# Optimization experiments

Measured on AMD Instinct MI355X. Metric: run time of the kernel, lower is better.

## Reference

```python
import jax, jax.numpy as jnp
import numpy as np

OUT_F, IN_F, RANK = 4096, 4096, 32
N_TOK = 8192  # batch 4 * seq 2048, flattened


def setup_inputs() -> dict:
    key = jax.random.key(0)
    k_x, k_w, k_s, k_a, k_b, k_bias = jax.random.split(key, 6)
    x = jax.random.normal(k_x, (N_TOK, IN_F), dtype=jnp.float32)
    # ternary weights in {-1, 0, +1}, stored as int8 buffer
    weight_q = (jax.random.randint(k_w, (OUT_F, IN_F), 0, 3) - 1).astype(jnp.int8)
    # per-output-channel absmean scale, shape [out, 1], positive
    scale = 0.02 + 0.05 * jax.random.uniform(k_s, (OUT_F, 1), dtype=jnp.float32)
    lora_A = 0.01 * jax.random.normal(k_a, (OUT_F, RANK), dtype=jnp.float32)
    lora_B = 0.01 * jax.random.normal(k_b, (RANK, IN_F), dtype=jnp.float32)
    bias = 0.01 * jax.random.normal(k_bias, (OUT_F,), dtype=jnp.float32)
    return {"x": x, "weight_q": weight_q, "scale": scale,
            "lora_A": lora_A, "lora_B": lora_B, "bias": bias}


def reference(x, weight_q, scale, lora_A, lora_B, bias):
    # out = (x @ W_q^T) * scale_per_out_channel + x @ B^T @ A^T + bias
    Wq = weight_q.astype(x.dtype)                       # dequantize {-1,0,1}
    out = jnp.einsum('ti,oi->to', x, Wq) * scale.reshape(1, -1)
    # low-rank LoRA residual: (x @ B^T) @ A^T, rank-RANK bottleneck
    out = out + (x @ lora_B.T) @ lora_A.T
    out = out + bias
    return out
```

## Files before the change

kernel.cpp:

```cpp
#include <hip/hip_runtime.h>
#include <stdint.h>

typedef unsigned short u16;
typedef __attribute__((ext_vector_type(8))) __bf16 bf16x8;
typedef __attribute__((ext_vector_type(4))) float f32x4;

__device__ __forceinline__ u16 f2bf(float f) {
  unsigned int u = __builtin_bit_cast(unsigned int, f);
  u = (u + 0x7FFFu + ((u >> 16) & 1u)) >> 16;
  return (u16)u;
}
__device__ __forceinline__ u16 tern2bf(int s) {
  return s == 0 ? (u16)0 : (s > 0 ? (u16)0x3F80 : (u16)0xBF80);
}

#define GLOAD_LDS16(g, l)                                                          \
  __builtin_amdgcn_global_load_lds((__attribute__((address_space(1))) void*)(g),   \
                                   (__attribute__((address_space(3))) void*)(l),   \
                                   16, 0, 0)

#define M_TOK 8192
#define N_OUT 4096
#define K_IN  4096
#define RANK  32

#define WS_XB    0ull
#define WS_WB    67108864ull
#define WS_BB    100663296ull
#define WS_A32   100925440ull
#define WS_T32   101187584ull
#define WS_TPART 101711872ull
#define WS_FLAG  110100480ull

__global__ void k_convert_x(const float4* __restrict__ x, ushort4* __restrict__ xb, int n4) {
  int stride = gridDim.x * blockDim.x;
  for (int i = blockIdx.x * blockDim.x + threadIdx.x; i < n4; i += stride) {
    float4 v = x[i];
    ushort4 o;
    o.x = f2bf(v.x); o.y = f2bf(v.y); o.z = f2bf(v.z); o.w = f2bf(v.w);
    xb[i] = o;
  }
}

__global__ void k_detect_wtype(const int* __restrict__ w, int* __restrict__ flag) {
  int v = w[threadIdx.x];
  bool ok = (v >= -1 && v <= 1);
  unsigned long long m = __ballot(ok);
  if (threadIdx.x == 0) *flag = (m == ~0ull) ? 1 : 0;
}

__global__ void k_convert_w(const void* __restrict__ wq, const int* __restrict__ flag,
                            ushort4* __restrict__ wb, int n4) {
  int is32 = *flag;
  int stride = gridDim.x * blockDim.x;
  for (int i = blockIdx.x * blockDim.x + threadIdx.x; i < n4; i += stride) {
    int s0, s1, s2, s3;
    if (is32) {
      int4 c = ((const int4*)wq)[i];
      s0 = c.x; s1 = c.y; s2 = c.z; s3 = c.w;
    } else {
      char4 c = ((const char4*)wq)[i];
      s0 = c.x; s1 = c.y; s2 = c.z; s3 = c.w;
    }
    ushort4 o;
    o.x = tern2bf(s0); o.y = tern2bf(s1); o.z = tern2bf(s2); o.w = tern2bf(s3);
    wb[i] = o;
  }
}

__global__ void k_prep_B(const float* __restrict__ loraB, u16* __restrict__ bb) {
  int idx = blockIdx.x * blockDim.x + threadIdx.x;
  if (idx < RANK * K_IN) bb[idx] = f2bf(loraB[idx]);
}

__global__ void k_prep_A(const float* __restrict__ loraA, const float* __restrict__ scale,
                         u16* __restrict__ a32) {
  int idx = blockIdx.x * blockDim.x + threadIdx.x;
  if (idx >= N_OUT * RANK) return;
  int o = idx >> 5;
  a32[idx] = f2bf(loraA[idx] / scale[o]);
}

__global__ __launch_bounds__(256) void k_lora_T(const u16* __restrict__ xb,
                                                const u16* __restrict__ bb,
                                                float* __restrict__ tpart) {
  __shared__ u16 As[256 * 32];
  __shared__ u16 Bs[32 * 32];
  int mt = blockIdx.x >> 3;
  int ks = blockIdx.x & 7;
  int tid = threadIdx.x, lane = tid & 63, wave = tid >> 6;
  int m0 = mt * 256;
  int kbase0 = ks * 512;
  f32x4 acc[4][2] = {};
  for (int step = 0; step < 16; ++step) {
    int kb = kbase0 + step * 32;
    __syncthreads();
#pragma unroll
    for (int i = 0; i < 4; ++i) {
      const u16* src = xb + (size_t)(m0 + i * 64 + (tid >> 2)) * K_IN + kb + (tid & 3) * 8;
      GLOAD_LDS16(src, &As[i * 2048 + tid * 8]);
    }
    if (tid < 128) {
      const u16* src = bb + (size_t)(tid >> 2) * K_IN + kb + (tid & 3) * 8;
      GLOAD_LDS16(src, &Bs[tid * 8]);
    }
    __syncthreads();
    bf16x8 b[2];
#pragma unroll
    for (int ni = 0; ni < 2; ++ni)
      b[ni] = *(const bf16x8*)&Bs[(ni * 16 + (lane & 15)) * 32 + (lane >> 4) * 8];
#pragma unroll
    for (int mi = 0; mi < 4; ++mi) {
      bf16x8 a = *(const bf16x8*)&As[(wave * 64 + mi * 16 + (lane & 15)) * 32 + (lane >> 4) * 8];
      acc[mi][0] = __builtin_amdgcn_mfma_f32_16x16x32_bf16(a, b[0], acc[mi][0], 0, 0, 0);
      acc[mi][1] = __builtin_amdgcn_mfma_f32_16x16x32_bf16(a, b[1], acc[mi][1], 0, 0, 0);
    }
  }
#pragma unroll
  for (int mi = 0; mi < 4; ++mi)
#pragma unroll
    for (int ni = 0; ni < 2; ++ni)
#pragma unroll
      for (int r = 0; r < 4; ++r) {
        int row = m0 + wave * 64 + mi * 16 + (lane >> 4) * 4 + r;
        int col = ni * 16 + (lane & 15);
        tpart[((size_t)ks * M_TOK + row) * RANK + col] = acc[mi][ni][r];
      }
}

__global__ void k_reduce_T(const float* __restrict__ tpart, u16* __restrict__ t32) {
  int idx = blockIdx.x * blockDim.x + threadIdx.x;
  if (idx >= M_TOK * RANK) return;
  int t = idx >> 5, r = idx & 31;
  float v = 0.f;
#pragma unroll
  for (int s = 0; s < 8; ++s) v += tpart[((size_t)s * M_TOK + t) * RANK + r];
  t32[idx] = f2bf(v);
}

__global__ __launch_bounds__(512, 2) void k_gemm8(const u16* __restrict__ xb,
                                                  const u16* __restrict__ wb,
                                                  const u16* __restrict__ t32,
                                                  const u16* __restrict__ a32,
                                                  const float* __restrict__ scale,
                                                  const float* __restrict__ bias,
                                                  float* __restrict__ out) {
  __shared__ u16 As[4][8192];
  __shared__ u16 Bs[4][8192];
  const int tid = threadIdx.x;
  const int l = tid & 63, w = tid >> 6;
  const int wm = w >> 2, wn = w & 3;
  const int bid = blockIdx.x;
  const int swz = (bid & 7) * 64 + (bid >> 3);
  const int m0 = (swz >> 4) * 256, n0 = (swz & 15) * 256;

  const int srow0 = (w * 2 + 0) * 16 + (l >> 2);
  const int srow1 = (w * 2 + 1) * 16 + (l >> 2);
  const int scx = ((l & 3) ^ ((l >> 3) & 3)) * 8;
  const int ldst0 = (w * 2 + 0) * 512 + l * 8;
  const int ldst1 = (w * 2 + 1) * 512 + l * 8;
  const int r15 = l & 15;
  const int cxr = (((l >> 4) ^ ((r15 >> 1) & 3)) * 8);

  f32x4 acc[8][4] = {};

  u16* AsF = &As[0][0];
  u16* BsF = &Bs[0][0];
  const u16* axs0 = xb + (size_t)(m0 + srow0) * K_IN + scx;
  const u16* axs1 = xb + (size_t)(m0 + srow1) * K_IN + scx;
  const u16* bxs0 = wb + (size_t)(n0 + srow0) * K_IN + scx;
  const u16* bxs1 = wb + (size_t)(n0 + srow1) * K_IN + scx;

#pragma unroll
  for (int ts = 0; ts < 3; ++ts) {
    GLOAD_LDS16(axs0 + ts * 32, AsF + ts * 8192 + ldst0);
    GLOAD_LDS16(axs1 + ts * 32, AsF + ts * 8192 + ldst1);
    GLOAD_LDS16(bxs0 + ts * 32, BsF + ts * 8192 + ldst0);
    GLOAD_LDS16(bxs1 + ts * 32, BsF + ts * 8192 + ldst1);
  }
  asm volatile("s_waitcnt vmcnt(8)" ::: "memory");
  asm volatile("s_barrier" ::: "memory");

  const int abase = (wm * 128 + r15) * 32 + cxr;
  const int bbase = (wn * 64 + r15) * 32 + cxr;

  const u16* ap0 = axs0 + 96;
  const u16* ap1 = axs1 + 96;
  const u16* bp0 = bxs0 + 96;
  const u16* bp1 = bxs1 + 96;

#define TILE(SLOT, STAGE_A, STAGE_B, WAIT, BAR)                                     \
  {                                                                                 \
    const u16* Asl = AsF + (SLOT) * 8192;                                           \
    const u16* Bsl = BsF + (SLOT) * 8192;                                           \
    bf16x8 a0[4], bfr[4], a1[4];                                                    \
    _Pragma("unroll") for (int mi = 0; mi < 4; ++mi)                                \
        a0[mi] = *(const bf16x8*)&Asl[abase + mi * 512];                            \
    _Pragma("unroll") for (int nj = 0; nj < 4; ++nj)                                \
        bfr[nj] = *(const bf16x8*)&Bsl[bbase + nj * 512];                           \
    STAGE_A                                                                         \
    __builtin_amdgcn_s_setprio(1);                                                  \
    _Pragma("unroll") for (int mi = 0; mi < 4; ++mi)                                \
    _Pragma("unroll") for (int nj = 0; nj < 4; ++nj)                                \
        acc[mi][nj] =                                                               \
            __builtin_amdgcn_mfma_f32_16x16x32_bf16(a0[mi], bfr[nj], acc[mi][nj], 0, 0, 0); \
    __builtin_amdgcn_s_setprio(0);                                                  \
    _Pragma("unroll") for (int mi = 0; mi < 4; ++mi)                                \
        a1[mi] = *(const bf16x8*)&Asl[abase + 2048 + mi * 512];                     \
    STAGE_B                                                                         \
    WAIT                                                                            \
    __builtin_amdgcn_s_setprio(1);                                                  \
    _Pragma("unroll") for (int mi = 0; mi < 4; ++mi)                                \
    _Pragma("unroll") for (int nj = 0; nj < 4; ++nj)                                \
        acc[4 + mi][nj] =                                                           \
            __builtin_amdgcn_mfma_f32_16x16x32_bf16(a1[mi], bfr[nj], acc[4 + mi][nj], 0, 0, 0); \
    __builtin_amdgcn_s_setprio(0);                                                  \
    BAR                                                                             \
  }

#define SA(DST)                                                                     \
  { GLOAD_LDS16(ap0, AsF + (DST) * 8192 + ldst0);                                   \
    GLOAD_LDS16(ap1, AsF + (DST) * 8192 + ldst1); }
#define SB(DST)                                                                     \
  { GLOAD_LDS16(bp0, BsF + (DST) * 8192 + ldst0);                                   \
    GLOAD_LDS16(bp1, BsF + (DST) * 8192 + ldst1);                                   \
    ap0 += 32; ap1 += 32; bp0 += 32; bp1 += 32; }
#define W8  asm volatile("s_waitcnt vmcnt(8)" ::: "memory");
#define W4  asm volatile("s_waitcnt vmcnt(4)" ::: "memory");
#define W0  asm volatile("s_waitcnt vmcnt(0)" ::: "memory");
#define BARR asm volatile("s_barrier" ::: "memory");

#pragma unroll 1
  for (int t = 0; t < 124; t += 4) {
    TILE(0, SA(3), SB(3), W8, BARR)
    TILE(1, SA(0), SB(0), W8, BARR)
    TILE(2, SA(1), SB(1), W8, BARR)
    TILE(3, SA(2), SB(2), W8, BARR)
  }
  TILE(0, SA(3), SB(3), W8, BARR)
  {
    const u16* la0 = t32 + (size_t)(m0 + srow0) * RANK + scx;
    const u16* la1 = t32 + (size_t)(m0 + srow1) * RANK + scx;
    const u16* lb0 = a32 + (size_t)(n0 + srow0) * RANK + scx;
    const u16* lb1 = a32 + (size_t)(n0 + srow1) * RANK + scx;
    TILE(1,
         { GLOAD_LDS16(la0, AsF + 0 * 8192 + ldst0); GLOAD_LDS16(la1, AsF + 0 * 8192 + ldst1); },
         { GLOAD_LDS16(lb0, BsF + 0 * 8192 + ldst0); GLOAD_LDS16(lb1, BsF + 0 * 8192 + ldst1); },
         W8, BARR)
  }
  TILE(2, , , W4, BARR)
  TILE(3, , , W0, BARR)
  TILE(0, , , , )

#pragma unroll
  for (int nj = 0; nj < 4; ++nj) {
    int col = n0 + wn * 64 + nj * 16 + r15;
    float s = scale[col], bv = bias[col];
#pragma unroll
    for (int fi = 0; fi < 8; ++fi) {
      int row = m0 + wm * 128 + (fi >> 2) * 64 + (fi & 3) * 16 + (l >> 4) * 4;
#pragma unroll
      for (int r = 0; r < 4; ++r)
        out[(size_t)(row + r) * N_OUT + col] = acc[fi][nj][r] * s + bv;
    }
  }
}

extern "C" void kernel_launch(void* const* d_in, const int* in_sizes, int n_in,
                              void* d_out, int out_size, void* d_ws, size_t ws_size,
                              hipStream_t stream) {
  const float* x     = (const float*)d_in[0];
  const void*  wq    = d_in[1];
  const float* scale = (const float*)d_in[2];
  const float* loraA = (const float*)d_in[3];
  const float* loraB = (const float*)d_in[4];
  const float* bias  = (const float*)d_in[5];
  float* out = (float*)d_out;

  char* ws = (char*)d_ws;
  u16*   xb    = (u16*)(ws + WS_XB);
  u16*   wbuf  = (u16*)(ws + WS_WB);
  u16*   bb    = (u16*)(ws + WS_BB);
  u16*   a32   = (u16*)(ws + WS_A32);
  u16*   t32   = (u16*)(ws + WS_T32);
  float* tpart = (float*)(ws + WS_TPART);
  int*   flag  = (int*)(ws + WS_FLAG);

  k_convert_x<<<2048, 256, 0, stream>>>((const float4*)x, (ushort4*)xb, M_TOK * K_IN / 4);
  k_detect_wtype<<<1, 64, 0, stream>>>((const int*)wq, flag);
  k_convert_w<<<2048, 256, 0, stream>>>(wq, flag, (ushort4*)wbuf, N_OUT * K_IN / 4);
  k_prep_B<<<512, 256, 0, stream>>>(loraB, bb);
  k_prep_A<<<512, 256, 0, stream>>>(loraA, scale, a32);
  k_lora_T<<<256, 256, 0, stream>>>(xb, bb, tpart);
  k_reduce_T<<<1024, 256, 0, stream>>>(tpart, t32);
  k_gemm8<<<512, 512, 0, stream>>>(xb, wbuf, t32, a32, scale, bias, out);

  (void)in_sizes; (void)n_in; (void)out_size; (void)ws_size;
}
```

Measured before the change: 325.8 us.

## Load weight B fragments directly into registers, bypassing LDS staging

The weight operand is no longer staged through shared memory. Each wave reads its B fragments straight from global memory into registers, double-buffered one tile ahead, and only the activation tile still goes through the four-slot LDS ring. This halves LDS capacity and traffic and removes the B-side LDS reads, which may allow more occupancy. In exchange, each wave issues its own uncoalesced 16-byte global loads, so waves that share an n-tile duplicate weight fetches, and register pressure rises along with a more fragile vmcnt accounting.

```diff
diff --git a/kernel.cpp b/kernel.cpp
--- a/kernel.cpp
+++ b/kernel.cpp
@@ -146,7 +146,6 @@
                                                   const float* __restrict__ bias,
                                                   float* __restrict__ out) {
   __shared__ u16 As[4][8192];
-  __shared__ u16 Bs[4][8192];
   const int tid = threadIdx.x;
   const int l = tid & 63, w = tid >> 6;
   const int wm = w >> 2, wn = w & 3;
@@ -165,92 +164,93 @@
   f32x4 acc[8][4] = {};
 
   u16* AsF = &As[0][0];
-  u16* BsF = &Bs[0][0];
   const u16* axs0 = xb + (size_t)(m0 + srow0) * K_IN + scx;
   const u16* axs1 = xb + (size_t)(m0 + srow1) * K_IN + scx;
-  const u16* bxs0 = wb + (size_t)(n0 + srow0) * K_IN + scx;
-  const u16* bxs1 = wb + (size_t)(n0 + srow1) * K_IN + scx;
+
+  const u16* wrowp[4];
+#pragma unroll
+  for (int nj = 0; nj < 4; ++nj)
+    wrowp[nj] = wb + (size_t)(n0 + wn * 64 + nj * 16 + r15) * K_IN + (l >> 4) * 8;
+  const u16* arowp[4];
+#pragma unroll
+  for (int nj = 0; nj < 4; ++nj)
+    arowp[nj] = a32 + (size_t)(n0 + wn * 64 + nj * 16 + r15) * RANK + (l >> 4) * 8;
+
+  bf16x8 bA[4], bB[4];
 
 #pragma unroll
   for (int ts = 0; ts < 3; ++ts) {
     GLOAD_LDS16(axs0 + ts * 32, AsF + ts * 8192 + ldst0);
     GLOAD_LDS16(axs1 + ts * 32, AsF + ts * 8192 + ldst1);
-    GLOAD_LDS16(bxs0 + ts * 32, BsF + ts * 8192 + ldst0);
-    GLOAD_LDS16(bxs1 + ts * 32, BsF + ts * 8192 + ldst1);
-  }
-  asm volatile("s_waitcnt vmcnt(8)" ::: "memory");
+  }
+#pragma unroll
+  for (int nj = 0; nj < 4; ++nj) { bA[nj] = *(const bf16x8*)(wrowp[nj]); wrowp[nj] += 32; }
+  asm volatile("s_waitcnt vmcnt(4)" ::: "memory");
   asm volatile("s_barrier" ::: "memory");
 
   const int abase = (wm * 128 + r15) * 32 + cxr;
-  const int bbase = (wn * 64 + r15) * 32 + cxr;
 
   const u16* ap0 = axs0 + 96;
   const u16* ap1 = axs1 + 96;
-  const u16* bp0 = bxs0 + 96;
-  const u16* bp1 = bxs1 + 96;
-
-#define TILE(SLOT, STAGE_A, STAGE_B, WAIT, BAR)                                     \
+
+#define SA(DST)                                                                     \
+  { GLOAD_LDS16(ap0, AsF + (DST) * 8192 + ldst0);                                   \
+    GLOAD_LDS16(ap1, AsF + (DST) * 8192 + ldst1);                                   \
+    ap0 += 32; ap1 += 32; }
+#define LOADB_W(BN)                                                                 \
+  { _Pragma("unroll") for (int nj = 0; nj < 4; ++nj) {                              \
+      BN[nj] = *(const bf16x8*)(wrowp[nj]); wrowp[nj] += 32; } }
+#define LOADB_L(BN)                                                                 \
+  { _Pragma("unroll") for (int nj = 0; nj < 4; ++nj) BN[nj] = *(const bf16x8*)(arowp[nj]); }
+#define W12 asm volatile("s_waitcnt vmcnt(12)" ::: "memory");
+#define W10 asm volatile("s_waitcnt vmcnt(10)" ::: "memory");
+#define W8  asm volatile("s_waitcnt vmcnt(8)" ::: "memory");
+#define BARR asm volatile("s_barrier" ::: "memory");
+
+#define TILE(SLOT, BC, LOADB, STAGE, WAIT, BAR)                                     \
   {                                                                                 \
     const u16* Asl = AsF + (SLOT) * 8192;                                           \
-    const u16* Bsl = BsF + (SLOT) * 8192;                                           \
-    bf16x8 a0[4], bfr[4], a1[4];                                                    \
+    bf16x8 a0[4], a1[4];                                                            \
     _Pragma("unroll") for (int mi = 0; mi < 4; ++mi)                                \
         a0[mi] = *(const bf16x8*)&Asl[abase + mi * 512];                            \
-    _Pragma("unroll") for (int nj = 0; nj < 4; ++nj)                                \
-        bfr[nj] = *(const bf16x8*)&Bsl[bbase + nj * 512];                           \
-    STAGE_A                                                                         \
+    LOADB                                                                           \
+    STAGE                                                                           \
     __builtin_amdgcn_s_setprio(1);                                                  \
     _Pragma("unroll") for (int mi = 0; mi < 4; ++mi)                                \
     _Pragma("unroll") for (int nj = 0; nj < 4; ++nj)                                \
         acc[mi][nj] =                                                               \
-            __builtin_amdgcn_mfma_f32_16x16x32_bf16(a0[mi], bfr[nj], acc[mi][nj], 0, 0, 0); \
+            __builtin_amdgcn_mfma_f32_16x16x32_bf16(a0[mi], BC[nj], acc[mi][nj], 0, 0, 0); \
     __builtin_amdgcn_s_setprio(0);                                                  \
     _Pragma("unroll") for (int mi = 0; mi < 4; ++mi)                                \
         a1[mi] = *(const bf16x8*)&Asl[abase + 2048 + mi * 512];                     \
-    STAGE_B                                                                         \
-    WAIT                                                                            \
     __builtin_amdgcn_s_setprio(1);                                                  \
     _Pragma("unroll") for (int mi = 0; mi < 4; ++mi)                                \
     _Pragma("unroll") for (int nj = 0; nj < 4; ++nj)                                \
         acc[4 + mi][nj] =                                                           \
-            __builtin_amdgcn_mfma_f32_16x16x32_bf16(a1[mi], bfr[nj], acc[4 + mi][nj], 0, 0, 0); \
+            __builtin_amdgcn_mfma_f32_16x16x32_bf16(a1[mi], BC[nj], acc[4 + mi][nj], 0, 0, 0); \
     __builtin_amdgcn_s_setprio(0);                                                  \
+    WAIT                                                                            \
     BAR                                                                             \
   }
-
-#define SA(DST)                                                                     \
-  { GLOAD_LDS16(ap0, AsF + (DST) * 8192 + ldst0);                                   \
-    GLOAD_LDS16(ap1, AsF + (DST) * 8192 + ldst1); }
-#define SB(DST)                                                                     \
-  { GLOAD_LDS16(bp0, BsF + (DST) * 8192 + ldst0);                                   \
-    GLOAD_LDS16(bp1, BsF + (DST) * 8192 + ldst1);                                   \
-    ap0 += 32; ap1 += 32; bp0 += 32; bp1 += 32; }
-#define W8  asm volatile("s_waitcnt vmcnt(8)" ::: "memory");
-#define W4  asm volatile("s_waitcnt vmcnt(4)" ::: "memory");
-#define W0  asm volatile("s_waitcnt vmcnt(0)" ::: "memory");
-#define BARR asm volatile("s_barrier" ::: "memory");
 
 #pragma unroll 1
   for (int t = 0; t < 124; t += 4) {
-    TILE(0, SA(3), SB(3), W8, BARR)
-    TILE(1, SA(0), SB(0), W8, BARR)
-    TILE(2, SA(1), SB(1), W8, BARR)
-    TILE(3, SA(2), SB(2), W8, BARR)
-  }
-  TILE(0, SA(3), SB(3), W8, BARR)
+    TILE(0, bA, LOADB_W(bB), SA(3), W12, BARR)
+    TILE(1, bB, LOADB_W(bA), SA(0), W12, BARR)
+    TILE(2, bA, LOADB_W(bB), SA(1), W12, BARR)
+    TILE(3, bB, LOADB_W(bA), SA(2), W12, BARR)
+  }
+  TILE(0, bA, LOADB_W(bB), SA(3), W12, BARR)
   {
     const u16* la0 = t32 + (size_t)(m0 + srow0) * RANK + scx;
     const u16* la1 = t32 + (size_t)(m0 + srow1) * RANK + scx;
-    const u16* lb0 = a32 + (size_t)(n0 + srow0) * RANK + scx;
-    const u16* lb1 = a32 + (size_t)(n0 + srow1) * RANK + scx;
-    TILE(1,
+    TILE(1, bB, LOADB_W(bA),
          { GLOAD_LDS16(la0, AsF + 0 * 8192 + ldst0); GLOAD_LDS16(la1, AsF + 0 * 8192 + ldst1); },
-         { GLOAD_LDS16(lb0, BsF + 0 * 8192 + ldst0); GLOAD_LDS16(lb1, BsF + 0 * 8192 + ldst1); },
-         W8, BARR)
-  }
-  TILE(2, , , W4, BARR)
-  TILE(3, , , W0, BARR)
-  TILE(0, , , , )
+         W12, BARR)
+  }
+  TILE(2, bA, LOADB_W(bB), , W10, BARR)
+  TILE(3, bB, LOADB_L(bA), , W8, BARR)
+  TILE(0, bA, , , , )
 
 #pragma unroll
   for (int nj = 0; nj < 4; ++nj) {
```

Result: slower. 439.3 us (+34.8%).

## Prefetch next tile's LDS fragments into registers before barrier

Applied to the files above, without the earlier changes.

Restructures the 4-stage LDS ring loop so each tile's first A fragments and B fragments are read from LDS for the next slot at the end of the current tile, after the vmcnt wait and before the barrier. The loads are double-buffered in even/odd register sets. The waitcnt thresholds are retuned to vmcnt(4), and pointer increments are split per operand. The aim is to hide LDS read latency behind the preceding MFMA work. In exchange it uses more VGPRs, which may lower occupancy, and requires careful slot-hazard ordering in the ring.

```diff
diff --git a/kernel.cpp b/kernel.cpp
--- a/kernel.cpp
+++ b/kernel.cpp
@@ -178,7 +178,7 @@
     GLOAD_LDS16(bxs0 + ts * 32, BsF + ts * 8192 + ldst0);
     GLOAD_LDS16(bxs1 + ts * 32, BsF + ts * 8192 + ldst1);
   }
-  asm volatile("s_waitcnt vmcnt(8)" ::: "memory");
+  asm volatile("s_waitcnt vmcnt(4)" ::: "memory");
   asm volatile("s_barrier" ::: "memory");
 
   const int abase = (wm * 128 + r15) * 32 + cxr;
@@ -189,68 +189,74 @@
   const u16* bp0 = bxs0 + 96;
   const u16* bp1 = bxs1 + 96;
 
-#define TILE(SLOT, STAGE_A, STAGE_B, WAIT, BAR)                                     \
+#define SA(DST)                                                                     \
+  { GLOAD_LDS16(ap0, AsF + (DST) * 8192 + ldst0);                                   \
+    GLOAD_LDS16(ap1, AsF + (DST) * 8192 + ldst1);                                   \
+    ap0 += 32; ap1 += 32; }
+#define SB(DST)                                                                     \
+  { GLOAD_LDS16(bp0, BsF + (DST) * 8192 + ldst0);                                   \
+    GLOAD_LDS16(bp1, BsF + (DST) * 8192 + ldst1);                                   \
+    bp0 += 32; bp1 += 32; }
+#define W4  asm volatile("s_waitcnt vmcnt(4)" ::: "memory");
+#define W0  asm volatile("s_waitcnt vmcnt(0)" ::: "memory");
+#define BARR asm volatile("s_barrier" ::: "memory");
+#define READN(NS, A0N, BN)                                                          \
+  { const u16* An = AsF + (NS) * 8192;                                              \
+    const u16* Bn = BsF + (NS) * 8192;                                              \
+    _Pragma("unroll") for (int mi = 0; mi < 4; ++mi)                                \
+        A0N[mi] = *(const bf16x8*)&An[abase + mi * 512];                            \
+    _Pragma("unroll") for (int nj = 0; nj < 4; ++nj)                                \
+        BN[nj] = *(const bf16x8*)&Bn[bbase + nj * 512]; }
+
+#define TILE(SLOT, A0C, BC, STAGE_A, STAGE_B, WAIT, RD, BAR)                        \
   {                                                                                 \
     const u16* Asl = AsF + (SLOT) * 8192;                                           \
-    const u16* Bsl = BsF + (SLOT) * 8192;                                           \
-    bf16x8 a0[4], bfr[4], a1[4];                                                    \
+    bf16x8 a1[4];                                                                   \
     _Pragma("unroll") for (int mi = 0; mi < 4; ++mi)                                \
-        a0[mi] = *(const bf16x8*)&Asl[abase + mi * 512];                            \
-    _Pragma("unroll") for (int nj = 0; nj < 4; ++nj)                                \
-        bfr[nj] = *(const bf16x8*)&Bsl[bbase + nj * 512];                           \
+        a1[mi] = *(const bf16x8*)&Asl[abase + 2048 + mi * 512];                     \
     STAGE_A                                                                         \
     __builtin_amdgcn_s_setprio(1);                                                  \
     _Pragma("unroll") for (int mi = 0; mi < 4; ++mi)                                \
     _Pragma("unroll") for (int nj = 0; nj < 4; ++nj)                                \
         acc[mi][nj] =                                                               \
-            __builtin_amdgcn_mfma_f32_16x16x32_bf16(a0[mi], bfr[nj], acc[mi][nj], 0, 0, 0); \
+            __builtin_amdgcn_mfma_f32_16x16x32_bf16(A0C[mi], BC[nj], acc[mi][nj], 0, 0, 0); \
     __builtin_amdgcn_s_setprio(0);                                                  \
-    _Pragma("unroll") for (int mi = 0; mi < 4; ++mi)                                \
-        a1[mi] = *(const bf16x8*)&Asl[abase + 2048 + mi * 512];                     \
     STAGE_B                                                                         \
-    WAIT                                                                            \
     __builtin_amdgcn_s_setprio(1);                                                  \
     _Pragma("unroll") for (int mi = 0; mi < 4; ++mi)                                \
     _Pragma("unroll") for (int nj = 0; nj < 4; ++nj)                                \
         acc[4 + mi][nj] =                                                           \
-            __builtin_amdgcn_mfma_f32_16x16x32_bf16(a1[mi], bfr[nj], acc[4 + mi][nj], 0, 0, 0); \
+            __builtin_amdgcn_mfma_f32_16x16x32_bf16(a1[mi], BC[nj], acc[4 + mi][nj], 0, 0, 0); \
     __builtin_amdgcn_s_setprio(0);                                                  \
+    WAIT                                                                            \
+    RD                                                                              \
     BAR                                                                             \
   }
 
-#define SA(DST)                                                                     \
-  { GLOAD_LDS16(ap0, AsF + (DST) * 8192 + ldst0);                                   \
-    GLOAD_LDS16(ap1, AsF + (DST) * 8192 + ldst1); }
-#define SB(DST)                                                                     \
-  { GLOAD_LDS16(bp0, BsF + (DST) * 8192 + ldst0);                                   \
-    GLOAD_LDS16(bp1, BsF + (DST) * 8192 + ldst1);                                   \
-    ap0 += 32; ap1 += 32; bp0 += 32; bp1 += 32; }
-#define W8  asm volatile("s_waitcnt vmcnt(8)" ::: "memory");
-#define W4  asm volatile("s_waitcnt vmcnt(4)" ::: "memory");
-#define W0  asm volatile("s_waitcnt vmcnt(0)" ::: "memory");
-#define BARR asm volatile("s_barrier" ::: "memory");
+  bf16x8 a0e[4], be[4], a0o[4], bo[4];
+  READN(0, a0e, be)
 
 #pragma unroll 1
   for (int t = 0; t < 124; t += 4) {
-    TILE(0, SA(3), SB(3), W8, BARR)
-    TILE(1, SA(0), SB(0), W8, BARR)
-    TILE(2, SA(1), SB(1), W8, BARR)
-    TILE(3, SA(2), SB(2), W8, BARR)
-  }
-  TILE(0, SA(3), SB(3), W8, BARR)
+    TILE(0, a0e, be, SA(3), SB(3), W4, READN(1, a0o, bo), BARR)
+    TILE(1, a0o, bo, SA(0), SB(0), W4, READN(2, a0e, be), BARR)
+    TILE(2, a0e, be, SA(1), SB(1), W4, READN(3, a0o, bo), BARR)
+    TILE(3, a0o, bo, SA(2), SB(2), W4, READN(0, a0e, be), BARR)
+  }
+  TILE(0, a0e, be, SA(3), SB(3), W4, READN(1, a0o, bo), BARR)
   {
     const u16* la0 = t32 + (size_t)(m0 + srow0) * RANK + scx;
     const u16* la1 = t32 + (size_t)(m0 + srow1) * RANK + scx;
     const u16* lb0 = a32 + (size_t)(n0 + srow0) * RANK + scx;
     const u16* lb1 = a32 + (size_t)(n0 + srow1) * RANK + scx;
-    TILE(1,
+    TILE(1, a0o, bo,
          { GLOAD_LDS16(la0, AsF + 0 * 8192 + ldst0); GLOAD_LDS16(la1, AsF + 0 * 8192 + ldst1); },
          { GLOAD_LDS16(lb0, BsF + 0 * 8192 + ldst0); GLOAD_LDS16(lb1, BsF + 0 * 8192 + ldst1); },
-         W8, BARR)
-  }
-  TILE(2, , , W4, BARR)
-  TILE(3, , , W0, BARR)
-  TILE(0, , , , )
+         W4, READN(2, a0e, be), BARR)
+  }
+  TILE(2, a0e, be, , , W0, READN(3, a0o, bo), BARR)
+  TILE(3, a0o, bo, , , , READN(0, a0e, be), BARR)
+  TILE(0, a0e, be, , , , , )
 
 #pragma unroll
   for (int nj = 0; nj < 4; ++nj) {
```

Result: no change. 323.3 us (-0.8%).

## Split each K-tile into two barrier-separated phases with explicit LDS waits

Applied to the files above, without the earlier changes.

The per-tile body becomes two phases (PHA and PHB), each ending its LDS fragment loads with an explicit lgkmcnt(0) wait and surrounded by workgroup barriers. This is meant to make waves in the block issue their MFMA bursts in lockstep, in the style of ping-pong scheduling, and to cut register pressure by reusing a single fa/fb fragment set. The cost is extra barriers per tile (four instead of one), which may add stalls and reduce how much LDS reads overlap with MFMA.

```diff
diff --git a/kernel.cpp b/kernel.cpp
--- a/kernel.cpp
+++ b/kernel.cpp
@@ -189,68 +189,81 @@
   const u16* bp0 = bxs0 + 96;
   const u16* bp1 = bxs1 + 96;
 
-#define TILE(SLOT, STAGE_A, STAGE_B, WAIT, BAR)                                     \
-  {                                                                                 \
-    const u16* Asl = AsF + (SLOT) * 8192;                                           \
-    const u16* Bsl = BsF + (SLOT) * 8192;                                           \
-    bf16x8 a0[4], bfr[4], a1[4];                                                    \
-    _Pragma("unroll") for (int mi = 0; mi < 4; ++mi)                                \
-        a0[mi] = *(const bf16x8*)&Asl[abase + mi * 512];                            \
-    _Pragma("unroll") for (int nj = 0; nj < 4; ++nj)                                \
-        bfr[nj] = *(const bf16x8*)&Bsl[bbase + nj * 512];                           \
-    STAGE_A                                                                         \
-    __builtin_amdgcn_s_setprio(1);                                                  \
-    _Pragma("unroll") for (int mi = 0; mi < 4; ++mi)                                \
-    _Pragma("unroll") for (int nj = 0; nj < 4; ++nj)                                \
-        acc[mi][nj] =                                                               \
-            __builtin_amdgcn_mfma_f32_16x16x32_bf16(a0[mi], bfr[nj], acc[mi][nj], 0, 0, 0); \
-    __builtin_amdgcn_s_setprio(0);                                                  \
-    _Pragma("unroll") for (int mi = 0; mi < 4; ++mi)                                \
-        a1[mi] = *(const bf16x8*)&Asl[abase + 2048 + mi * 512];                     \
-    STAGE_B                                                                         \
-    WAIT                                                                            \
-    __builtin_amdgcn_s_setprio(1);                                                  \
-    _Pragma("unroll") for (int mi = 0; mi < 4; ++mi)                                \
-    _Pragma("unroll") for (int nj = 0; nj < 4; ++nj)                                \
-        acc[4 + mi][nj] =                                                           \
-            __builtin_amdgcn_mfma_f32_16x16x32_bf16(a1[mi], bfr[nj], acc[4 + mi][nj], 0, 0, 0); \
-    __builtin_amdgcn_s_setprio(0);                                                  \
-    BAR                                                                             \
-  }
+  bf16x8 fa[4], fb[4];
 
 #define SA(DST)                                                                     \
   { GLOAD_LDS16(ap0, AsF + (DST) * 8192 + ldst0);                                   \
-    GLOAD_LDS16(ap1, AsF + (DST) * 8192 + ldst1); }
+    GLOAD_LDS16(ap1, AsF + (DST) * 8192 + ldst1);                                   \
+    ap0 += 32; ap1 += 32; }
 #define SB(DST)                                                                     \
   { GLOAD_LDS16(bp0, BsF + (DST) * 8192 + ldst0);                                   \
     GLOAD_LDS16(bp1, BsF + (DST) * 8192 + ldst1);                                   \
-    ap0 += 32; ap1 += 32; bp0 += 32; bp1 += 32; }
+    bp0 += 32; bp1 += 32; }
 #define W8  asm volatile("s_waitcnt vmcnt(8)" ::: "memory");
 #define W4  asm volatile("s_waitcnt vmcnt(4)" ::: "memory");
 #define W0  asm volatile("s_waitcnt vmcnt(0)" ::: "memory");
 #define BARR asm volatile("s_barrier" ::: "memory");
+#define LGKM0 asm volatile("s_waitcnt lgkmcnt(0)" ::: "memory");
+#define MM0(mi, nj)                                                                 \
+  acc[mi][nj] = __builtin_amdgcn_mfma_f32_16x16x32_bf16(fa[mi], fb[nj], acc[mi][nj], 0, 0, 0);
+#define MM1(mi, nj)                                                                 \
+  acc[4 + (mi)][nj] =                                                               \
+      __builtin_amdgcn_mfma_f32_16x16x32_bf16(fa[mi], fb[nj], acc[4 + (mi)][nj], 0, 0, 0);
+
+#define PHA(SLOT, STAGE)                                                            \
+  {                                                                                 \
+    const u16* Asl = AsF + (SLOT) * 8192;                                           \
+    const u16* Bsl = BsF + (SLOT) * 8192;                                           \
+    _Pragma("unroll") for (int mi = 0; mi < 4; ++mi)                                \
+        fa[mi] = *(const bf16x8*)&Asl[abase + mi * 512];                            \
+    _Pragma("unroll") for (int nj = 0; nj < 4; ++nj)                                \
+        fb[nj] = *(const bf16x8*)&Bsl[bbase + nj * 512];                            \
+    STAGE                                                                           \
+    BARR                                                                            \
+    LGKM0                                                                           \
+    __builtin_amdgcn_s_setprio(1);                                                  \
+    MM0(0, 0) MM0(0, 1) MM0(0, 2) MM0(0, 3) MM0(1, 0) MM0(1, 1) MM0(1, 2) MM0(1, 3) \
+    MM0(2, 0) MM0(2, 1) MM0(2, 2) MM0(2, 3) MM0(3, 0) MM0(3, 1) MM0(3, 2) MM0(3, 3) \
+    __builtin_amdgcn_s_setprio(0);                                                  \
+    BARR                                                                            \
+  }
+
+#define PHB(SLOT, STAGE, WAIT)                                                      \
+  {                                                                                 \
+    const u16* Asl = AsF + (SLOT) * 8192;                                           \
+    _Pragma("unroll") for (int mi = 0; mi < 4; ++mi)                                \
+        fa[mi] = *(const bf16x8*)&Asl[abase + 2048 + mi * 512];                     \
+    STAGE                                                                           \
+    WAIT                                                                            \
+    BARR                                                                            \
+    LGKM0                                                                           \
+    __builtin_amdgcn_s_setprio(1);                                                  \
+    MM1(0, 0) MM1(0, 1) MM1(0, 2) MM1(0, 3) MM1(1, 0) MM1(1, 1) MM1(1, 2) MM1(1, 3) \
+    MM1(2, 0) MM1(2, 1) MM1(2, 2) MM1(2, 3) MM1(3, 0) MM1(3, 1) MM1(3, 2) MM1(3, 3) \
+    __builtin_amdgcn_s_setprio(0);                                                  \
+    BARR                                                                            \
+  }
 
 #pragma unroll 1
   for (int t = 0; t < 124; t += 4) {
-    TILE(0, SA(3), SB(3), W8, BARR)
-    TILE(1, SA(0), SB(0), W8, BARR)
-    TILE(2, SA(1), SB(1), W8, BARR)
-    TILE(3, SA(2), SB(2), W8, BARR)
-  }
-  TILE(0, SA(3), SB(3), W8, BARR)
+    PHA(0, SA(3)) PHB(0, SB(3), W8)
+    PHA(1, SA(0)) PHB(1, SB(0), W8)
+    PHA(2, SA(1)) PHB(2, SB(1), W8)
+    PHA(3, SA(2)) PHB(3, SB(2), W8)
+  }
+  PHA(0, SA(3)) PHB(0, SB(3), W8)
   {
     const u16* la0 = t32 + (size_t)(m0 + srow0) * RANK + scx;
     const u16* la1 = t32 + (size_t)(m0 + srow1) * RANK + scx;
     const u16* lb0 = a32 + (size_t)(n0 + srow0) * RANK + scx;
     const u16* lb1 = a32 + (size_t)(n0 + srow1) * RANK + scx;
-    TILE(1,
-         { GLOAD_LDS16(la0, AsF + 0 * 8192 + ldst0); GLOAD_LDS16(la1, AsF + 0 * 8192 + ldst1); },
-         { GLOAD_LDS16(lb0, BsF + 0 * 8192 + ldst0); GLOAD_LDS16(lb1, BsF + 0 * 8192 + ldst1); },
-         W8, BARR)
-  }
-  TILE(2, , , W4, BARR)
-  TILE(3, , , W0, BARR)
-  TILE(0, , , , )
+    PHA(1, { GLOAD_LDS16(la0, AsF + 0 * 8192 + ldst0); GLOAD_LDS16(la1, AsF + 0 * 8192 + ldst1); })
+    PHB(1, { GLOAD_LDS16(lb0, BsF + 0 * 8192 + ldst0); GLOAD_LDS16(lb1, BsF + 0 * 8192 + ldst1); },
+        W8)
+  }
+  PHA(2, ) PHB(2, , W4)
+  PHA(3, ) PHB(3, , W0)
+  PHA(0, ) PHB(0, , )
 
 #pragma unroll
   for (int nj = 0; nj < 4; ++nj) {
```

Measured after the change: 340.1 us. 1.04x slower.
